# Optimization experiments

Measured on AMD Instinct MI355X. Metric: run time of the kernel, lower is better.

The kernel has to match this reference:

```python
import jax, jax.numpy as jnp
import numpy as np

EPS = 1e-12  # torch F.normalize eps

def _l2norm(v, axis):
    n = jnp.sqrt(jnp.sum(v * v, axis=axis, keepdims=True))
    return v / jnp.maximum(n, EPS)

def setup_inputs() -> dict:
    key = jax.random.key(0)
    k1, k2 = jax.random.split(key)
    B, N, D, K = 8, 2048, 128, 64
    x = jax.random.normal(k1, (B, N, D), dtype=jnp.float32)
    std1 = 1.0 / np.sqrt(K * D)
    centroids = jax.random.uniform(k2, (K, D), dtype=jnp.float32, minval=-std1, maxval=std1)
    return {"x": x, "centroids": centroids}

def reference(x, centroids):
    # x: [B, N, D], centroids: [K, D]
    B, N, D = x.shape
    K = centroids.shape[0]
    xn = _l2norm(x, axis=-1)                       # descriptor-wise L2 normalize
    res = xn[:, :, None, :] - centroids[None, None]  # [B, N, K, D]
    dist = jnp.sum(res * res, axis=-1)             # [B, N, K] squared distances
    assign = jax.nn.softmax(dist, axis=-1)         # softmax over clusters (NOTE: positive distances, as in source)
    vlad = jnp.einsum('bnk,bnkd->bkd', assign, res)  # weighted residual sum over N
    vlad = _l2norm(vlad, axis=2)                   # intra-normalization per cluster
    vlad = vlad.reshape(B, K * D)
    vlad = _l2norm(vlad, axis=1)                   # global L2 normalize
    return vlad
```

## Files before the change

kernel.cpp:

```cpp
#include <hip/hip_runtime.h>
#include <math.h>

#define BB 8
#define NN 2048
#define DD 128
#define KK 64
#define PP 128
#define NPB (NN / PP)

__global__ __launch_bounds__(256, 4) void netvlad_k1(
    const float* __restrict__ x, const float* __restrict__ cent,
    float* __restrict__ part_acc, float* __restrict__ part_sA)
{
    const int b    = blockIdx.x >> 7;
    const int p    = blockIdx.x & 127;
    const int t    = threadIdx.x;
    const int kq   = t >> 3;
    const int pr   = t & 7;
    const int dbase = pr * 16;
    const int wave = t >> 6;

    __shared__ __align__(16) float xs[NPB][DD];
    __shared__ __align__(16) float sL[NPB][4];

    int off[4];
    #pragma unroll
    for (int jj = 0; jj < 4; ++jj) off[jj] = dbase + (((jj + pr) & 3) << 2);

    const int i0 = t >> 4, tl = t & 15;
    const float* xr = x + ((size_t)b * NN + (size_t)p * NPB + i0) * DD;
    float4 v0 = *(const float4*)(xr + tl * 4);
    float4 v1 = *(const float4*)(xr + 64 + tl * 4);

    float4 cA[4], cB[4];
    float cn2a = 0.f, cn2b = 0.f;
    #pragma unroll
    for (int jj = 0; jj < 4; ++jj) {
        cA[jj] = *(const float4*)(cent + (2 * kq) * DD + off[jj]);
        cB[jj] = *(const float4*)(cent + (2 * kq + 1) * DD + off[jj]);
        cn2a += cA[jj].x*cA[jj].x + cA[jj].y*cA[jj].y + cA[jj].z*cA[jj].z + cA[jj].w*cA[jj].w;
        cn2b += cB[jj].x*cB[jj].x + cB[jj].y*cB[jj].y + cB[jj].z*cB[jj].z + cB[jj].w*cB[jj].w;
    }
    #pragma unroll
    for (int m = 1; m < 8; m <<= 1) {
        cn2a += __shfl_xor(cn2a, m);
        cn2b += __shfl_xor(cn2b, m);
    }

    {
        float ss = v0.x*v0.x + v0.y*v0.y + v0.z*v0.z + v0.w*v0.w
                 + v1.x*v1.x + v1.y*v1.y + v1.z*v1.z + v1.w*v1.w;
        #pragma unroll
        for (int m = 1; m < 16; m <<= 1) ss += __shfl_xor(ss, m);
        const float rn = 1.0f / fmaxf(sqrtf(ss), 1e-12f);
        v0.x *= rn; v0.y *= rn; v0.z *= rn; v0.w *= rn;
        v1.x *= rn; v1.y *= rn; v1.z *= rn; v1.w *= rn;
        *(float4*)(&xs[i0][tl * 4])      = v0;
        *(float4*)(&xs[i0][64 + tl * 4]) = v1;
    }
    __syncthreads();

    float e0[NPB], e1[NPB];
    #pragma unroll
    for (int i = 0; i < NPB; ++i) {
        float S0 = 0.f, S1 = 0.f;
        #pragma unroll
        for (int jj = 0; jj < 4; ++jj) {
            float4 v = *(const float4*)(&xs[i][off[jj]]);
            S0 += v.x*cA[jj].x + v.y*cA[jj].y + v.z*cA[jj].z + v.w*cA[jj].w;
            S1 += v.x*cB[jj].x + v.y*cB[jj].y + v.z*cB[jj].z + v.w*cB[jj].w;
        }
        #pragma unroll
        for (int m = 1; m < 8; m <<= 1) {
            S0 += __shfl_xor(S0, m);
            S1 += __shfl_xor(S1, m);
        }
        e0[i] = __expf(cn2a - 2.f * S0);
        e1[i] = __expf(cn2b - 2.f * S1);
        float es = e0[i] + e1[i];
        #pragma unroll
        for (int m = 8; m < 64; m <<= 1) es += __shfl_xor(es, m);
        if ((t & 63) == 0) sL[i][wave] = es;
    }
    __syncthreads();

    float4 acc0[4], acc1[4];
    #pragma unroll
    for (int jj = 0; jj < 4; ++jj) {
        acc0[jj] = make_float4(0.f, 0.f, 0.f, 0.f);
        acc1[jj] = make_float4(0.f, 0.f, 0.f, 0.f);
    }
    float sA0 = 0.f, sA1 = 0.f;
    #pragma unroll
    for (int i = 0; i < NPB; ++i) {
        const float4 s4 = *(const float4*)(&sL[i][0]);
        const float rs = 1.0f / (s4.x + s4.y + s4.z + s4.w);
        const float a0 = e0[i] * rs, a1 = e1[i] * rs;
        sA0 += a0; sA1 += a1;
        #pragma unroll
        for (int jj = 0; jj < 4; ++jj) {
            float4 v = *(const float4*)(&xs[i][off[jj]]);
            acc0[jj].x += a0*v.x; acc0[jj].y += a0*v.y; acc0[jj].z += a0*v.z; acc0[jj].w += a0*v.w;
            acc1[jj].x += a1*v.x; acc1[jj].y += a1*v.y; acc1[jj].z += a1*v.z; acc1[jj].w += a1*v.w;
        }
    }

    const size_t base = (size_t)(b * PP + p) * KK * DD;
    #pragma unroll
    for (int jj = 0; jj < 4; ++jj) {
        *(float4*)(part_acc + base + (2 * kq) * DD + off[jj])     = acc0[jj];
        *(float4*)(part_acc + base + (2 * kq + 1) * DD + off[jj]) = acc1[jj];
    }
    if (pr == 0) {
        part_sA[(b * PP + p) * KK + 2 * kq]     = sA0;
        part_sA[(b * PP + p) * KK + 2 * kq + 1] = sA1;
    }
}

__global__ __launch_bounds__(128) void netvlad_k2(
    const float* __restrict__ cent, const float* __restrict__ part_acc,
    const float* __restrict__ part_sA, float* __restrict__ out)
{
    const int b  = blockIdx.x >> 6;
    const int k  = blockIdx.x & 63;
    const int t  = threadIdx.x;
    const int d4 = t & 31;
    const int ps = t >> 5;

    __shared__ float sAL[2];
    {
        float sA = part_sA[(b * PP + t) * KK + k];
        #pragma unroll
        for (int m = 1; m < 64; m <<= 1) sA += __shfl_xor(sA, m);
        if ((t & 63) == 0) sAL[t >> 6] = sA;
    }

    float4 acc = make_float4(0.f, 0.f, 0.f, 0.f);
    const float* base = part_acc + ((size_t)(b * PP) * KK + k) * DD + d4 * 4;
    #pragma unroll 8
    for (int pp = 0; pp < 32; ++pp) {
        const float4 v = *(const float4*)(base + (size_t)(ps * 32 + pp) * KK * DD);
        acc.x += v.x; acc.y += v.y; acc.z += v.z; acc.w += v.w;
    }

    __shared__ float4 red[4][32];
    red[ps][d4] = acc;
    __syncthreads();
    const float sAt = sAL[0] + sAL[1];

    if (t < 32) {
        float4 v = red[0][t];
        #pragma unroll
        for (int s = 1; s < 4; ++s) {
            v.x += red[s][t].x; v.y += red[s][t].y;
            v.z += red[s][t].z; v.w += red[s][t].w;
        }
        const float4 c = *(const float4*)(cent + k * DD + t * 4);
        v.x -= c.x * sAt; v.y -= c.y * sAt; v.z -= c.z * sAt; v.w -= c.w * sAt;

        float ss = v.x*v.x + v.y*v.y + v.z*v.z + v.w*v.w;
        #pragma unroll
        for (int m = 1; m < 32; m <<= 1) ss += __shfl_xor(ss, m);
        const float rn = 0.125f / fmaxf(sqrtf(ss), 1e-12f);
        v.x *= rn; v.y *= rn; v.z *= rn; v.w *= rn;
        *(float4*)(out + ((size_t)b * KK + k) * DD + t * 4) = v;
    }
}

extern "C" void kernel_launch(void* const* d_in, const int* in_sizes, int n_in,
                              void* d_out, int out_size, void* d_ws, size_t ws_size,
                              hipStream_t stream) {
    const float* x    = (const float*)d_in[0];
    const float* cent = (const float*)d_in[1];
    float* out = (float*)d_out;

    char* ws = (char*)d_ws;
    float* part_sA  = (float*)ws;
    float* part_acc = (float*)(ws + (1 << 19));

    netvlad_k1<<<dim3(BB * PP), dim3(256), 0, stream>>>(x, cent, part_acc, part_sA);
    netvlad_k2<<<dim3(BB * KK), dim3(128), 0, stream>>>(cent, part_acc, part_sA, out);
}
```

Measured before the change: 92.58 us.

## Halve partial-sum blocks, tile points in two halves, fold centroid subtraction into k1

Each k1 block now handles 32 points instead of 16, processed in two tiles of 16, so the partial accumulator buffer written to and read from global memory is halved. The per-cluster assignment-weighted centroid term is subtracted inside k1, which removes the separate part_sA buffer and its reduction in k2. k2 now sums 64 partials with 256 threads. The trade-off is half as many k1 blocks (512) with a lower occupancy hint, which gives less parallelism and latency hiding in the main kernel.

```diff
diff --git a/kernel.cpp b/kernel.cpp
--- a/kernel.cpp
+++ b/kernel.cpp
@@ -5,32 +5,38 @@
 #define NN 2048
 #define DD 128
 #define KK 64
-#define PP 128
+#define PP 64
 #define NPB (NN / PP)
+#define TI 16
 
-__global__ __launch_bounds__(256, 4) void netvlad_k1(
+__global__ __launch_bounds__(256, 2) void netvlad_k1(
     const float* __restrict__ x, const float* __restrict__ cent,
-    float* __restrict__ part_acc, float* __restrict__ part_sA)
+    float* __restrict__ part_acc)
 {
-    const int b    = blockIdx.x >> 7;
-    const int p    = blockIdx.x & 127;
+    const int b    = blockIdx.x >> 6;
+    const int p    = blockIdx.x & 63;
     const int t    = threadIdx.x;
     const int kq   = t >> 3;
     const int pr   = t & 7;
     const int dbase = pr * 16;
     const int wave = t >> 6;
 
-    __shared__ __align__(16) float xs[NPB][DD];
-    __shared__ __align__(16) float sL[NPB][4];
+    __shared__ __align__(16) float xs[2][TI][DD];
+    __shared__ __align__(16) float sL[2][TI][4];
 
     int off[4];
     #pragma unroll
     for (int jj = 0; jj < 4; ++jj) off[jj] = dbase + (((jj + pr) & 3) << 2);
 
     const int i0 = t >> 4, tl = t & 15;
-    const float* xr = x + ((size_t)b * NN + (size_t)p * NPB + i0) * DD;
-    float4 v0 = *(const float4*)(xr + tl * 4);
-    float4 v1 = *(const float4*)(xr + 64 + tl * 4);
+    const float* xb = x + ((size_t)b * NN + (size_t)p * NPB) * DD;
+    float4 xv[2][2];
+    #pragma unroll
+    for (int tt = 0; tt < 2; ++tt) {
+        const float* xr = xb + (size_t)(tt * TI + i0) * DD;
+        xv[tt][0] = *(const float4*)(xr + tl * 4);
+        xv[tt][1] = *(const float4*)(xr + 64 + tl * 4);
+    }
 
     float4 cA[4], cB[4];
     float cn2a = 0.f, cn2b = 0.f;
@@ -47,43 +53,6 @@
         cn2b += __shfl_xor(cn2b, m);
     }
 
-    {
-        float ss = v0.x*v0.x + v0.y*v0.y + v0.z*v0.z + v0.w*v0.w
-                 + v1.x*v1.x + v1.y*v1.y + v1.z*v1.z + v1.w*v1.w;
-        #pragma unroll
-        for (int m = 1; m < 16; m <<= 1) ss += __shfl_xor(ss, m);
-        const float rn = 1.0f / fmaxf(sqrtf(ss), 1e-12f);
-        v0.x *= rn; v0.y *= rn; v0.z *= rn; v0.w *= rn;
-        v1.x *= rn; v1.y *= rn; v1.z *= rn; v1.w *= rn;
-        *(float4*)(&xs[i0][tl * 4])      = v0;
-        *(float4*)(&xs[i0][64 + tl * 4]) = v1;
-    }
-    __syncthreads();
-
-    float e0[NPB], e1[NPB];
-    #pragma unroll
-    for (int i = 0; i < NPB; ++i) {
-        float S0 = 0.f, S1 = 0.f;
-        #pragma unroll
-        for (int jj = 0; jj < 4; ++jj) {
-            float4 v = *(const float4*)(&xs[i][off[jj]]);
-            S0 += v.x*cA[jj].x + v.y*cA[jj].y + v.z*cA[jj].z + v.w*cA[jj].w;
-            S1 += v.x*cB[jj].x + v.y*cB[jj].y + v.z*cB[jj].z + v.w*cB[jj].w;
-        }
-        #pragma unroll
-        for (int m = 1; m < 8; m <<= 1) {
-            S0 += __shfl_xor(S0, m);
-            S1 += __shfl_xor(S1, m);
-        }
-        e0[i] = __expf(cn2a - 2.f * S0);
-        e1[i] = __expf(cn2b - 2.f * S1);
-        float es = e0[i] + e1[i];
-        #pragma unroll
-        for (int m = 8; m < 64; m <<= 1) es += __shfl_xor(es, m);
-        if ((t & 63) == 0) sL[i][wave] = es;
-    }
-    __syncthreads();
-
     float4 acc0[4], acc1[4];
     #pragma unroll
     for (int jj = 0; jj < 4; ++jj) {
@@ -91,35 +60,76 @@
         acc1[jj] = make_float4(0.f, 0.f, 0.f, 0.f);
     }
     float sA0 = 0.f, sA1 = 0.f;
+
     #pragma unroll
-    for (int i = 0; i < NPB; ++i) {
-        const float4 s4 = *(const float4*)(&sL[i][0]);
-        const float rs = 1.0f / (s4.x + s4.y + s4.z + s4.w);
-        const float a0 = e0[i] * rs, a1 = e1[i] * rs;
-        sA0 += a0; sA1 += a1;
+    for (int tt = 0; tt < 2; ++tt) {
+        {
+            float4 v0 = xv[tt][0], v1 = xv[tt][1];
+            float ss = v0.x*v0.x + v0.y*v0.y + v0.z*v0.z + v0.w*v0.w
+                     + v1.x*v1.x + v1.y*v1.y + v1.z*v1.z + v1.w*v1.w;
+            #pragma unroll
+            for (int m = 1; m < 16; m <<= 1) ss += __shfl_xor(ss, m);
+            const float rn = 1.0f / fmaxf(sqrtf(ss), 1e-12f);
+            v0.x *= rn; v0.y *= rn; v0.z *= rn; v0.w *= rn;
+            v1.x *= rn; v1.y *= rn; v1.z *= rn; v1.w *= rn;
+            *(float4*)(&xs[tt][i0][tl * 4])      = v0;
+            *(float4*)(&xs[tt][i0][64 + tl * 4]) = v1;
+        }
+        __syncthreads();
+
+        float e0[TI], e1[TI];
         #pragma unroll
-        for (int jj = 0; jj < 4; ++jj) {
-            float4 v = *(const float4*)(&xs[i][off[jj]]);
-            acc0[jj].x += a0*v.x; acc0[jj].y += a0*v.y; acc0[jj].z += a0*v.z; acc0[jj].w += a0*v.w;
-            acc1[jj].x += a1*v.x; acc1[jj].y += a1*v.y; acc1[jj].z += a1*v.z; acc1[jj].w += a1*v.w;
+        for (int i = 0; i < TI; ++i) {
+            float S0 = 0.f, S1 = 0.f;
+            #pragma unroll
+            for (int jj = 0; jj < 4; ++jj) {
+                float4 v = *(const float4*)(&xs[tt][i][off[jj]]);
+                S0 += v.x*cA[jj].x + v.y*cA[jj].y + v.z*cA[jj].z + v.w*cA[jj].w;
+                S1 += v.x*cB[jj].x + v.y*cB[jj].y + v.z*cB[jj].z + v.w*cB[jj].w;
+            }
+            #pragma unroll
+            for (int m = 1; m < 8; m <<= 1) {
+                S0 += __shfl_xor(S0, m);
+                S1 += __shfl_xor(S1, m);
+            }
+            e0[i] = __expf(cn2a - 2.f * S0);
+            e1[i] = __expf(cn2b - 2.f * S1);
+            float es = e0[i] + e1[i];
+            #pragma unroll
+            for (int m = 8; m < 64; m <<= 1) es += __shfl_xor(es, m);
+            if ((t & 63) == 0) sL[tt][i][wave] = es;
+        }
+        __syncthreads();
+
+        #pragma unroll
+        for (int i = 0; i < TI; ++i) {
+            const float4 s4 = *(const float4*)(&sL[tt][i][0]);
+            const float rs = 1.0f / (s4.x + s4.y + s4.z + s4.w);
+            const float a0 = e0[i] * rs, a1 = e1[i] * rs;
+            sA0 += a0; sA1 += a1;
+            #pragma unroll
+            for (int jj = 0; jj < 4; ++jj) {
+                float4 v = *(const float4*)(&xs[tt][i][off[jj]]);
+                acc0[jj].x += a0*v.x; acc0[jj].y += a0*v.y; acc0[jj].z += a0*v.z; acc0[jj].w += a0*v.w;
+                acc1[jj].x += a1*v.x; acc1[jj].y += a1*v.y; acc1[jj].z += a1*v.z; acc1[jj].w += a1*v.w;
+            }
         }
     }
 
     const size_t base = (size_t)(b * PP + p) * KK * DD;
     #pragma unroll
     for (int jj = 0; jj < 4; ++jj) {
+        acc0[jj].x -= sA0 * cA[jj].x; acc0[jj].y -= sA0 * cA[jj].y;
+        acc0[jj].z -= sA0 * cA[jj].z; acc0[jj].w -= sA0 * cA[jj].w;
+        acc1[jj].x -= sA1 * cB[jj].x; acc1[jj].y -= sA1 * cB[jj].y;
+        acc1[jj].z -= sA1 * cB[jj].z; acc1[jj].w -= sA1 * cB[jj].w;
         *(float4*)(part_acc + base + (2 * kq) * DD + off[jj])     = acc0[jj];
         *(float4*)(part_acc + base + (2 * kq + 1) * DD + off[jj]) = acc1[jj];
     }
-    if (pr == 0) {
-        part_sA[(b * PP + p) * KK + 2 * kq]     = sA0;
-        part_sA[(b * PP + p) * KK + 2 * kq + 1] = sA1;
-    }
 }
 
-__global__ __launch_bounds__(128) void netvlad_k2(
-    const float* __restrict__ cent, const float* __restrict__ part_acc,
-    const float* __restrict__ part_sA, float* __restrict__ out)
+__global__ __launch_bounds__(256) void netvlad_k2(
+    const float* __restrict__ part_acc, float* __restrict__ out)
 {
     const int b  = blockIdx.x >> 6;
     const int k  = blockIdx.x & 63;
@@ -127,37 +137,25 @@
     const int d4 = t & 31;
     const int ps = t >> 5;
 
-    __shared__ float sAL[2];
-    {
-        float sA = part_sA[(b * PP + t) * KK + k];
-        #pragma unroll
-        for (int m = 1; m < 64; m <<= 1) sA += __shfl_xor(sA, m);
-        if ((t & 63) == 0) sAL[t >> 6] = sA;
-    }
-
     float4 acc = make_float4(0.f, 0.f, 0.f, 0.f);
     const float* base = part_acc + ((size_t)(b * PP) * KK + k) * DD + d4 * 4;
-    #pragma unroll 8
-    for (int pp = 0; pp < 32; ++pp) {
-        const float4 v = *(const float4*)(base + (size_t)(ps * 32 + pp) * KK * DD);
+    #pragma unroll
+    for (int pp = 0; pp < 8; ++pp) {
+        const float4 v = *(const float4*)(base + (size_t)(pp * 8 + ps) * KK * DD);
         acc.x += v.x; acc.y += v.y; acc.z += v.z; acc.w += v.w;
     }
 
-    __shared__ float4 red[4][32];
+    __shared__ __align__(16) float4 red[8][32];
     red[ps][d4] = acc;
     __syncthreads();
-    const float sAt = sAL[0] + sAL[1];
 
     if (t < 32) {
         float4 v = red[0][t];
         #pragma unroll
-        for (int s = 1; s < 4; ++s) {
+        for (int s = 1; s < 8; ++s) {
             v.x += red[s][t].x; v.y += red[s][t].y;
             v.z += red[s][t].z; v.w += red[s][t].w;
         }
-        const float4 c = *(const float4*)(cent + k * DD + t * 4);
-        v.x -= c.x * sAt; v.y -= c.y * sAt; v.z -= c.z * sAt; v.w -= c.w * sAt;
-
         float ss = v.x*v.x + v.y*v.y + v.z*v.z + v.w*v.w;
         #pragma unroll
         for (int m = 1; m < 32; m <<= 1) ss += __shfl_xor(ss, m);
@@ -174,10 +172,8 @@
     const float* cent = (const float*)d_in[1];
     float* out = (float*)d_out;
 
-    char* ws = (char*)d_ws;
-    float* part_sA  = (float*)ws;
-    float* part_acc = (float*)(ws + (1 << 19));
+    float* part_acc = (float*)d_ws;
 
-    netvlad_k1<<<dim3(BB * PP), dim3(256), 0, stream>>>(x, cent, part_acc, part_sA);
-    netvlad_k2<<<dim3(BB * KK), dim3(128), 0, stream>>>(cent, part_acc, part_sA, out);
+    netvlad_k1<<<dim3(BB * PP), dim3(256), 0, stream>>>(x, cent, part_acc);
+    netvlad_k2<<<dim3(BB * KK), dim3(256), 0, stream>>>(part_acc, out);
 }
```

After: 109.8 us. +18.6%, slower.

## Fold centroid subtraction into partial sums and widen reduction kernel

Applied to the files above, without the earlier changes.

The first kernel now subtracts sA*centroid from each partial accumulator before storing it, so the separate per-partition assignment-sum buffer and its reduction in the second kernel are no longer needed. The second kernel grows to 512 threads, with 16 slices each summing 8 partitions before a shared-memory reduction. This is meant to cut the small extra traffic and dependency work in the reduction, and to get more loads in flight per block. The subtraction adds a few FMAs per thread in the first kernel.

```diff
diff --git a/kernel.cpp b/kernel.cpp
--- a/kernel.cpp
+++ b/kernel.cpp
@@ -10,7 +10,7 @@
 
 __global__ __launch_bounds__(256, 4) void netvlad_k1(
     const float* __restrict__ x, const float* __restrict__ cent,
-    float* __restrict__ part_acc, float* __restrict__ part_sA)
+    float* __restrict__ part_acc)
 {
     const int b    = blockIdx.x >> 7;
     const int p    = blockIdx.x & 127;
@@ -108,18 +108,17 @@
     const size_t base = (size_t)(b * PP + p) * KK * DD;
     #pragma unroll
     for (int jj = 0; jj < 4; ++jj) {
+        acc0[jj].x -= sA0 * cA[jj].x; acc0[jj].y -= sA0 * cA[jj].y;
+        acc0[jj].z -= sA0 * cA[jj].z; acc0[jj].w -= sA0 * cA[jj].w;
+        acc1[jj].x -= sA1 * cB[jj].x; acc1[jj].y -= sA1 * cB[jj].y;
+        acc1[jj].z -= sA1 * cB[jj].z; acc1[jj].w -= sA1 * cB[jj].w;
         *(float4*)(part_acc + base + (2 * kq) * DD + off[jj])     = acc0[jj];
         *(float4*)(part_acc + base + (2 * kq + 1) * DD + off[jj]) = acc1[jj];
     }
-    if (pr == 0) {
-        part_sA[(b * PP + p) * KK + 2 * kq]     = sA0;
-        part_sA[(b * PP + p) * KK + 2 * kq + 1] = sA1;
-    }
 }
 
-__global__ __launch_bounds__(128) void netvlad_k2(
-    const float* __restrict__ cent, const float* __restrict__ part_acc,
-    const float* __restrict__ part_sA, float* __restrict__ out)
+__global__ __launch_bounds__(512) void netvlad_k2(
+    const float* __restrict__ part_acc, float* __restrict__ out)
 {
     const int b  = blockIdx.x >> 6;
     const int k  = blockIdx.x & 63;
@@ -127,37 +126,25 @@
     const int d4 = t & 31;
     const int ps = t >> 5;
 
-    __shared__ float sAL[2];
-    {
-        float sA = part_sA[(b * PP + t) * KK + k];
-        #pragma unroll
-        for (int m = 1; m < 64; m <<= 1) sA += __shfl_xor(sA, m);
-        if ((t & 63) == 0) sAL[t >> 6] = sA;
-    }
-
     float4 acc = make_float4(0.f, 0.f, 0.f, 0.f);
     const float* base = part_acc + ((size_t)(b * PP) * KK + k) * DD + d4 * 4;
-    #pragma unroll 8
-    for (int pp = 0; pp < 32; ++pp) {
-        const float4 v = *(const float4*)(base + (size_t)(ps * 32 + pp) * KK * DD);
+    #pragma unroll
+    for (int j = 0; j < 8; ++j) {
+        const float4 v = *(const float4*)(base + (size_t)(j * 16 + ps) * KK * DD);
         acc.x += v.x; acc.y += v.y; acc.z += v.z; acc.w += v.w;
     }
 
-    __shared__ float4 red[4][32];
+    __shared__ __align__(16) float4 red[16][32];
     red[ps][d4] = acc;
     __syncthreads();
-    const float sAt = sAL[0] + sAL[1];
 
     if (t < 32) {
         float4 v = red[0][t];
         #pragma unroll
-        for (int s = 1; s < 4; ++s) {
+        for (int s = 1; s < 16; ++s) {
             v.x += red[s][t].x; v.y += red[s][t].y;
             v.z += red[s][t].z; v.w += red[s][t].w;
         }
-        const float4 c = *(const float4*)(cent + k * DD + t * 4);
-        v.x -= c.x * sAt; v.y -= c.y * sAt; v.z -= c.z * sAt; v.w -= c.w * sAt;
-
         float ss = v.x*v.x + v.y*v.y + v.z*v.z + v.w*v.w;
         #pragma unroll
         for (int m = 1; m < 32; m <<= 1) ss += __shfl_xor(ss, m);
@@ -174,10 +161,8 @@
     const float* cent = (const float*)d_in[1];
     float* out = (float*)d_out;
 
-    char* ws = (char*)d_ws;
-    float* part_sA  = (float*)ws;
-    float* part_acc = (float*)(ws + (1 << 19));
+    float* part_acc = (float*)d_ws;
 
-    netvlad_k1<<<dim3(BB * PP), dim3(256), 0, stream>>>(x, cent, part_acc, part_sA);
-    netvlad_k2<<<dim3(BB * KK), dim3(128), 0, stream>>>(cent, part_acc, part_sA, out);
+    netvlad_k1<<<dim3(BB * PP), dim3(256), 0, stream>>>(x, cent, part_acc);
+    netvlad_k2<<<dim3(BB * KK), dim3(512), 0, stream>>>(part_acc, out);
 }
```

After: 111.9 us. +20.8%, slower.
